# Optimization experiments

Hardware: AMD Instinct MI355X
Metric: run time of the kernel (lower is better)

The kernel has to match this reference:

```python
import jax, jax.numpy as jnp
import numpy as np

N_HEAD = 16
N_EMBD = 64  # per-head dim in this module's convention
INNER = N_HEAD * N_EMBD  # 1024


def setup_inputs() -> dict:
    key = jax.random.key(0)
    ks = jax.random.split(key, 6)
    B, S = 4, 2048
    scale = 0.02
    return {
        "x": jax.random.normal(ks[0], (B, S, N_EMBD), dtype=jnp.float32),
        "Wq": jax.random.normal(ks[1], (N_EMBD, INNER), dtype=jnp.float32) * scale,
        "Wk": jax.random.normal(ks[2], (N_EMBD, INNER), dtype=jnp.float32) * scale,
        "Wv": jax.random.normal(ks[3], (N_EMBD, INNER), dtype=jnp.float32) * scale,
        "Wo": jax.random.normal(ks[4], (INNER, N_EMBD), dtype=jnp.float32) * scale,
        "bo": jax.random.normal(ks[5], (N_EMBD,), dtype=jnp.float32) * scale,
        "causal_mask": 1,
    }


def reference(x, Wq, Wk, Wv, Wo, bo, causal_mask):
    B, S, _ = x.shape
    # projections: [B,S,INNER] -> [B,H,S,D]
    def split_heads(t):
        return t.reshape(B, S, N_HEAD, N_EMBD).transpose(0, 2, 1, 3)
    q = split_heads(x @ Wq)
    k = split_heads(x @ Wk)
    v = split_heads(x @ Wv)
    # [B,H,S,S]
    scores = jnp.einsum("bhqd,bhkd->bhqk", q, k) / jnp.sqrt(jnp.float32(N_EMBD))
    if causal_mask:
        future = jnp.triu(jnp.ones((S, S), dtype=scores.dtype), k=1)
        scores = scores - 1e9 * future  # matches torch: subtract 1e9*mask
    attn = jax.nn.softmax(scores, axis=-1)
    out = jnp.einsum("bhqk,bhkd->bhqd", attn, v)
    out = out.transpose(0, 2, 1, 3).reshape(B, S, INNER)
    return out @ Wo + bo
```

## Files before the change

### kernel.cpp

```cpp
#include <hip/hip_runtime.h>
#include <hip/hip_bf16.h>

#define NHEAD 16
#define HDIM 64
#define DINNER 1024
#define NBATCH 4
#define SEQ 2048
#define NTOK (NBATCH*SEQ)

typedef __bf16 bf16;
typedef __bf16 bf16x4 __attribute__((ext_vector_type(4)));
typedef __bf16 bf16x8 __attribute__((ext_vector_type(8)));
typedef float f32x4 __attribute__((ext_vector_type(4)));

#define OFF_BO   8
#define OFF_WQT  128
#define OFF_WKT  (OFF_WQT + DINNER*HDIM)
#define OFF_WVT  (OFF_WKT + DINNER*HDIM)
#define OFF_WOT  (OFF_WVT + DINNER*HDIM)
#define OFF_Q    (OFF_WOT + DINNER*HDIM)
#define OFF_K    (OFF_Q + NTOK*DINNER)
#define OFF_VT   (OFF_K + NTOK*DINNER)
#define OFF_ATT  (OFF_VT + NTOK*DINNER)

#define SSCALE 0.18033688011112042f

static __device__ __forceinline__ bf16x8 ld8(const bf16* p) {
  return *reinterpret_cast<const bf16x8*>(p);
}
static __device__ __forceinline__ float ldw(const void* W, int i, int isbf) {
  return isbf ? (float)((const bf16*)W)[i] : ((const float*)W)[i];
}

static __device__ __forceinline__ int detect_isbf(const void* x, int tid,
                                                  int* sflag) {
  if (tid < 64) {
    const unsigned short* xb = (const unsigned short*)x;
    bool ok = true;
#pragma unroll
    for (int i = 0; i < 8; i++) {
      unsigned e = (xb[tid * 8 + i] >> 7) & 0xFF;
      ok = ok && (e >= 64 && e <= 140);
    }
    unsigned long long mball = __ballot(ok);
    if (tid == 0) *sflag = (mball == ~0ull) ? 1 : 0;
  }
  __syncthreads();
  return *sflag;
}

__global__ __launch_bounds__(256) void prep_kernel(
    const void* __restrict__ x, const void* __restrict__ Wq,
    const void* __restrict__ Wk, const void* __restrict__ Wv,
    const void* __restrict__ Wo, const void* __restrict__ bo,
    bf16* __restrict__ ws) {
  __shared__ int sflag;
  int isbf = detect_isbf(x, threadIdx.x, &sflag);
  int z = blockIdx.y;
  int idx = blockIdx.x * 256 + threadIdx.x;
  if (z < 3) {
    const void* src = (z == 0) ? Wq : (z == 1) ? Wk : Wv;
    bf16* dst = ws + ((z == 0) ? OFF_WQT : (z == 1) ? OFF_WKT : OFF_WVT);
    int d = idx >> 10, n = idx & 1023;
    float v = ldw(src, idx, isbf);
    if (z == 0) v *= SSCALE;
    dst[n * HDIM + d] = (bf16)v;
  } else if (z == 3) {
    int k = idx >> 6, n = idx & 63;
    ws[OFF_WOT + n * DINNER + k] = (bf16)ldw(Wo, idx, isbf);
  } else {
    if (idx < 64) ws[OFF_BO + idx] = (bf16)ldw(bo, idx, isbf);
  }
}

__global__ __launch_bounds__(256) void qkv_kernel(const void* __restrict__ x,
                                                  bf16* __restrict__ ws) {
  __shared__ __align__(16) bf16 Vst[4][16 * 72];
  __shared__ int sflag;
  int isbf = detect_isbf(x, threadIdx.x, &sflag);
  int tt = blockIdx.x;
  int w = threadIdx.x >> 6;
  int nc = blockIdx.y * 4 + w;
  int lane = threadIdx.x & 63;
  int lq = lane & 15, quad = lane >> 4;
  int n0 = nc * 64;
  bf16x8 wq0[4], wq1[4], wk0[4], wk1[4], wv0[4], wv1[4], ao0[4], ao1[4];
#pragma unroll
  for (int c = 0; c < 4; c++) {
    int n = n0 + c * 16 + lq;
    const bf16* r;
    r = ws + OFF_WQT + n * HDIM; wq0[c] = ld8(r + quad * 8); wq1[c] = ld8(r + 32 + quad * 8);
    r = ws + OFF_WKT + n * HDIM; wk0[c] = ld8(r + quad * 8); wk1[c] = ld8(r + 32 + quad * 8);
    r = ws + OFF_WVT + n * HDIM; wv0[c] = ld8(r + quad * 8); wv1[c] = ld8(r + 32 + quad * 8);
    const bf16* orow = ws + OFF_WOT + (size_t)(c * 16 + lq) * DINNER + n0;
    ao0[c] = ld8(orow + quad * 8); ao1[c] = ld8(orow + 32 + quad * 8);
  }
  bf16* Qb = ws + OFF_Q;
  bf16* Kb = ws + OFF_K;
  bf16* VTb = ws + OFF_VT;
#pragma unroll
  for (int mi = 0; mi < 4; mi++) {
    int t0 = tt * 64 + mi * 16;
    bf16x8 x0, x1;
    if (isbf) {
      const bf16* xr = (const bf16*)x + (size_t)(t0 + lq) * HDIM;
      x0 = ld8(xr + quad * 8);
      x1 = ld8(xr + 32 + quad * 8);
    } else {
      const float* xf = (const float*)x + (size_t)(t0 + lq) * HDIM;
      f32x4 a0 = *reinterpret_cast<const f32x4*>(xf + quad * 8);
      f32x4 a1 = *reinterpret_cast<const f32x4*>(xf + quad * 8 + 4);
      f32x4 b0 = *reinterpret_cast<const f32x4*>(xf + 32 + quad * 8);
      f32x4 b1 = *reinterpret_cast<const f32x4*>(xf + 32 + quad * 8 + 4);
#pragma unroll
      for (int j = 0; j < 4; j++) {
        x0[j] = (bf16)a0[j]; x0[4 + j] = (bf16)a1[j];
        x1[j] = (bf16)b0[j]; x1[4 + j] = (bf16)b1[j];
      }
    }
    int b = t0 >> 11, s0 = t0 & (SEQ - 1);
    size_t rowbase = ((size_t)(b * NHEAD + nc) * SEQ + s0 + lq) * HDIM;
#pragma unroll
    for (int c = 0; c < 4; c++) {
      f32x4 z = {0.f, 0.f, 0.f, 0.f};
      z = __builtin_amdgcn_mfma_f32_16x16x32_bf16(wq0[c], x0, z, 0, 0, 0);
      z = __builtin_amdgcn_mfma_f32_16x16x32_bf16(wq1[c], x1, z, 0, 0, 0);
      bf16x4 pk = {(bf16)z[0], (bf16)z[1], (bf16)z[2], (bf16)z[3]};
      *reinterpret_cast<bf16x4*>(&Qb[rowbase + c * 16 + quad * 4]) = pk;
    }
#pragma unroll
    for (int c = 0; c < 4; c++) {
      f32x4 z = {0.f, 0.f, 0.f, 0.f};
      z = __builtin_amdgcn_mfma_f32_16x16x32_bf16(wk0[c], x0, z, 0, 0, 0);
      z = __builtin_amdgcn_mfma_f32_16x16x32_bf16(wk1[c], x1, z, 0, 0, 0);
      bf16x4 pk = {(bf16)z[0], (bf16)z[1], (bf16)z[2], (bf16)z[3]};
      *reinterpret_cast<bf16x4*>(&Kb[rowbase + c * 16 + quad * 4]) = pk;
    }
#pragma unroll
    for (int c = 0; c < 4; c++) {
      f32x4 z = {0.f, 0.f, 0.f, 0.f};
      z = __builtin_amdgcn_mfma_f32_16x16x32_bf16(wv0[c], x0, z, 0, 0, 0);
      z = __builtin_amdgcn_mfma_f32_16x16x32_bf16(wv1[c], x1, z, 0, 0, 0);
      bf16x4 pk = {(bf16)z[0], (bf16)z[1], (bf16)z[2], (bf16)z[3]};
      *reinterpret_cast<bf16x4*>(&Vst[w][lq * 72 + c * 16 + quad * 4]) = pk;
    }
    bf16x8 bv0 = ld8(&Vst[w][lq * 72 + quad * 8]);
    bf16x8 bv1 = ld8(&Vst[w][lq * 72 + 32 + quad * 8]);
#pragma unroll
    for (int c = 0; c < 4; c++) {
      f32x4 z2 = {0.f, 0.f, 0.f, 0.f};
      z2 = __builtin_amdgcn_mfma_f32_16x16x32_bf16(ao0[c], bv0, z2, 0, 0, 0);
      z2 = __builtin_amdgcn_mfma_f32_16x16x32_bf16(ao1[c], bv1, z2, 0, 0, 0);
#pragma unroll
      for (int r = 0; r < 4; r++) {
        int d = c * 16 + quad * 4 + r;
        VTb[(((size_t)b * NHEAD + nc) * HDIM + d) * SEQ + s0 + lq] = (bf16)z2[r];
      }
    }
  }
}

__global__ __launch_bounds__(256, 2) void flash_kernel(const int* __restrict__ cmask,
                                                       bf16* __restrict__ ws) {
  __shared__ __align__(16) bf16 Kl[2][64 * 64];
  __shared__ __align__(16) bf16 Vl[2][64 * 64];
  __shared__ __align__(16) bf16 Pl[4][16 * 64];
  const int qmap[16] = {15,13,11,9,0,2,4,6,14,12,10,8,1,3,5,7};
  int bid = blockIdx.x;
  int bh = (bid & 7) * 8 + ((bid >> 3) & 7);
  int qt = qmap[bid >> 6];
  int w = threadIdx.x >> 6;
  int lane = threadIdx.x & 63;
  int lq = lane & 15, quad = lane >> 4;
  int causal = cmask[0];
  const bf16* Q = ws + OFF_Q + (size_t)bh * SEQ * HDIM;
  const bf16* K = ws + OFF_K + (size_t)bh * SEQ * HDIM;
  const bf16* VT = ws + OFF_VT + (size_t)bh * HDIM * SEQ;
  int b = bh >> 4, h = bh & 15;
  bf16* ar = ws + OFF_ATT;
  int sr = threadIdx.x >> 2;
  int sg = (threadIdx.x & 3) * 16;
  int sc0 = (((threadIdx.x & 3) * 2) ^ (sr & 7)) << 3;
  int sc1 = (((threadIdx.x & 3) * 2 + 1) ^ (sr & 7)) << 3;
  int rq0 = (quad ^ (lq & 7)) << 3;
  int rq1 = ((4 + quad) ^ (lq & 7)) << 3;

  int qb = qt * 128;
  int qw = qb + w * 32;
  int T = (causal ? (qb + 128) : SEQ) / 64;

  bf16x8 bq[2][2];
#pragma unroll
  for (int m = 0; m < 2; m++) {
    const bf16* qrow = Q + (qw + m * 16 + lq) * HDIM;
    bq[m][0] = ld8(qrow + quad * 8);
    bq[m][1] = ld8(qrow + 32 + quad * 8);
  }
  f32x4 o[2][4];
  float lsum[2] = {0.f, 0.f};
#pragma unroll
  for (int m = 0; m < 2; m++)
#pragma unroll
    for (int c = 0; c < 4; c++) o[m][c] = (f32x4){0.f, 0.f, 0.f, 0.f};

  bf16x8 kst0 = ld8(K + sr * HDIM + sg);
  bf16x8 kst1 = ld8(K + sr * HDIM + sg + 8);
  bf16x8 vst0 = ld8(VT + sr * SEQ + sg);
  bf16x8 vst1 = ld8(VT + sr * SEQ + sg + 8);

  for (int ti = 0; ti < T; ti++) {
    int buf = ti & 1;
    int k0 = ti * 64;
    *reinterpret_cast<bf16x8*>(&Kl[buf][sr * 64 + sc0]) = kst0;
    *reinterpret_cast<bf16x8*>(&Kl[buf][sr * 64 + sc1]) = kst1;
    *reinterpret_cast<bf16x8*>(&Vl[buf][sr * 64 + sc0]) = vst0;
    *reinterpret_cast<bf16x8*>(&Vl[buf][sr * 64 + sc1]) = vst1;
    int kn = (ti + 1 < T) ? (k0 + 64) : k0;
    kst0 = ld8(K + (kn + sr) * HDIM + sg);
    kst1 = ld8(K + (kn + sr) * HDIM + sg + 8);
    vst0 = ld8(VT + sr * SEQ + kn + sg);
    vst1 = ld8(VT + sr * SEQ + kn + sg + 8);
    __syncthreads();
    f32x4 st[2][4];
#pragma unroll
    for (int t = 0; t < 4; t++) {
      bf16x8 a0 = ld8(&Kl[buf][(t * 16 + lq) * 64 + rq0]);
      bf16x8 a1 = ld8(&Kl[buf][(t * 16 + lq) * 64 + rq1]);
#pragma unroll
      for (int m = 0; m < 2; m++) {
        f32x4 z = {0.f, 0.f, 0.f, 0.f};
        z = __builtin_amdgcn_mfma_f32_16x16x32_bf16(a0, bq[m][0], z, 0, 0, 0);
        z = __builtin_amdgcn_mfma_f32_16x16x32_bf16(a1, bq[m][1], z, 0, 0, 0);
        st[m][t] = z;
      }
    }
    bool needmask = causal && (k0 + 63 > qw);
    bf16x8 bp[2][2];
#pragma unroll
    for (int m = 0; m < 2; m++) {
      if (needmask) {
        int qrel = qw + m * 16 + lq - k0 - quad * 4;
#pragma unroll
        for (int t = 0; t < 4; t++)
#pragma unroll
          for (int r = 0; r < 4; r++)
            if (t * 16 + r > qrel) st[m][t][r] = -200.0f;
      }
      float sum = 0.f;
#pragma unroll
      for (int t = 0; t < 4; t++) {
        float e0 = exp2f(st[m][t][0]);
        float e1 = exp2f(st[m][t][1]);
        float e2 = exp2f(st[m][t][2]);
        float e3 = exp2f(st[m][t][3]);
        sum += (e0 + e1) + (e2 + e3);
        bf16x4 pk = {(bf16)e0, (bf16)e1, (bf16)e2, (bf16)e3};
        int ch = ((t * 2 + (quad >> 1)) ^ (lq & 7)) << 3;
        *reinterpret_cast<bf16x4*>(&Pl[w][lq * 64 + ch + (quad & 1) * 4]) = pk;
      }
      lsum[m] += sum;
      bp[m][0] = ld8(&Pl[w][lq * 64 + rq0]);
      bp[m][1] = ld8(&Pl[w][lq * 64 + rq1]);
    }
#pragma unroll
    for (int c = 0; c < 4; c++) {
      bf16x8 av0 = ld8(&Vl[buf][(c * 16 + lq) * 64 + rq0]);
      bf16x8 av1 = ld8(&Vl[buf][(c * 16 + lq) * 64 + rq1]);
#pragma unroll
      for (int m = 0; m < 2; m++) {
        o[m][c] = __builtin_amdgcn_mfma_f32_16x16x32_bf16(av0, bp[m][0], o[m][c], 0, 0, 0);
        o[m][c] = __builtin_amdgcn_mfma_f32_16x16x32_bf16(av1, bp[m][1], o[m][c], 0, 0, 0);
      }
    }
  }
#pragma unroll
  for (int m = 0; m < 2; m++) {
    lsum[m] += __shfl_xor(lsum[m], 16);
    lsum[m] += __shfl_xor(lsum[m], 32);
    float inv = 1.0f / lsum[m];
    size_t rowoff = ((size_t)(b * SEQ + qw + m * 16 + lq)) * DINNER + h * HDIM;
#pragma unroll
    for (int c = 0; c < 4; c++) {
      bf16x4 ov = {(bf16)(o[m][c][0] * inv), (bf16)(o[m][c][1] * inv),
                   (bf16)(o[m][c][2] * inv), (bf16)(o[m][c][3] * inv)};
      *reinterpret_cast<bf16x4*>(&ar[rowoff + c * 16 + quad * 4]) = ov;
    }
  }
}

__global__ __launch_bounds__(256) void reduce_kernel(const bf16* __restrict__ ws,
                                                     const void* __restrict__ x,
                                                     void* __restrict__ outp) {
  __shared__ int sflag;
  int isbf = detect_isbf(x, threadIdx.x, &sflag);
  int idx = blockIdx.x * 256 + threadIdx.x;
  int t = idx >> 6, d = idx & 63;
  const bf16* ar = ws + OFF_ATT + (size_t)t * DINNER + d;
  float s = (float)ws[OFF_BO + d];
#pragma unroll
  for (int h = 0; h < 16; h++) s += (float)ar[h * 64];
  if (isbf) ((bf16*)outp)[idx] = (bf16)s;
  else      ((float*)outp)[idx] = s;
}

extern "C" void kernel_launch(void* const* d_in, const int* in_sizes, int n_in,
                              void* d_out, int out_size, void* d_ws, size_t ws_size,
                              hipStream_t stream) {
  const void* x  = d_in[0];
  const void* Wq = d_in[1];
  const void* Wk = d_in[2];
  const void* Wv = d_in[3];
  const void* Wo = d_in[4];
  const void* bo = d_in[5];
  const int* cm  = (const int*)d_in[6];
  bf16* ws = (bf16*)d_ws;

  hipLaunchKernelGGL(prep_kernel, dim3(256, 5), dim3(256), 0, stream,
                     x, Wq, Wk, Wv, Wo, bo, ws);
  hipLaunchKernelGGL(qkv_kernel, dim3(128, 4), dim3(256), 0, stream, x, ws);
  hipLaunchKernelGGL(flash_kernel, dim3(1024), dim3(256), 0, stream, cm, ws);
  hipLaunchKernelGGL(reduce_kernel, dim3(2048), dim3(256), 0, stream, ws, x, d_out);
}
```

Before: 164.1 us.

## Restructure QKV projection: smaller token tiles, staged coalesced Q/K stores, fewer live weights

The QKV kernel now handles 32 tokens per block instead of 64, doubling the grid. It loads the weights for one projection at a time, so fewer registers stay live. Q and K tiles are staged through shared memory so each lane writes a full 16-byte chunk of a row, replacing the scattered 8-byte stores. The cost is more blocks that each reload the weights, plus extra LDS round-trips, in a kernel that is only part of the total runtime.

```diff
diff --git a/kernel.cpp b/kernel.cpp
--- a/kernel.cpp
+++ b/kernel.cpp
@@ -75,7 +75,7 @@
 
 __global__ __launch_bounds__(256) void qkv_kernel(const void* __restrict__ x,
                                                   bf16* __restrict__ ws) {
-  __shared__ __align__(16) bf16 Vst[4][16 * 72];
+  __shared__ __align__(16) bf16 St[4][16 * 72];
   __shared__ int sflag;
   int isbf = detect_isbf(x, threadIdx.x, &sflag);
   int tt = blockIdx.x;
@@ -84,77 +84,95 @@
   int lane = threadIdx.x & 63;
   int lq = lane & 15, quad = lane >> 4;
   int n0 = nc * 64;
-  bf16x8 wq0[4], wq1[4], wk0[4], wk1[4], wv0[4], wv1[4], ao0[4], ao1[4];
-#pragma unroll
-  for (int c = 0; c < 4; c++) {
-    int n = n0 + c * 16 + lq;
-    const bf16* r;
-    r = ws + OFF_WQT + n * HDIM; wq0[c] = ld8(r + quad * 8); wq1[c] = ld8(r + 32 + quad * 8);
-    r = ws + OFF_WKT + n * HDIM; wk0[c] = ld8(r + quad * 8); wk1[c] = ld8(r + 32 + quad * 8);
-    r = ws + OFF_WVT + n * HDIM; wv0[c] = ld8(r + quad * 8); wv1[c] = ld8(r + 32 + quad * 8);
-    const bf16* orow = ws + OFF_WOT + (size_t)(c * 16 + lq) * DINNER + n0;
-    ao0[c] = ld8(orow + quad * 8); ao1[c] = ld8(orow + 32 + quad * 8);
-  }
-  bf16* Qb = ws + OFF_Q;
-  bf16* Kb = ws + OFF_K;
-  bf16* VTb = ws + OFF_VT;
-#pragma unroll
-  for (int mi = 0; mi < 4; mi++) {
-    int t0 = tt * 64 + mi * 16;
-    bf16x8 x0, x1;
+  int t0 = tt * 32;
+  int b = t0 >> 11, s0 = t0 & (SEQ - 1);
+  bf16x8 xa[2], xb[2];
+#pragma unroll
+  for (int mi = 0; mi < 2; mi++) {
+    int trow = t0 + mi * 16 + lq;
     if (isbf) {
-      const bf16* xr = (const bf16*)x + (size_t)(t0 + lq) * HDIM;
-      x0 = ld8(xr + quad * 8);
-      x1 = ld8(xr + 32 + quad * 8);
+      const bf16* xr = (const bf16*)x + (size_t)trow * HDIM;
+      xa[mi] = ld8(xr + quad * 8);
+      xb[mi] = ld8(xr + 32 + quad * 8);
     } else {
-      const float* xf = (const float*)x + (size_t)(t0 + lq) * HDIM;
+      const float* xf = (const float*)x + (size_t)trow * HDIM;
       f32x4 a0 = *reinterpret_cast<const f32x4*>(xf + quad * 8);
       f32x4 a1 = *reinterpret_cast<const f32x4*>(xf + quad * 8 + 4);
       f32x4 b0 = *reinterpret_cast<const f32x4*>(xf + 32 + quad * 8);
       f32x4 b1 = *reinterpret_cast<const f32x4*>(xf + 32 + quad * 8 + 4);
 #pragma unroll
       for (int j = 0; j < 4; j++) {
-        x0[j] = (bf16)a0[j]; x0[4 + j] = (bf16)a1[j];
-        x1[j] = (bf16)b0[j]; x1[4 + j] = (bf16)b1[j];
-      }
-    }
-    int b = t0 >> 11, s0 = t0 & (SEQ - 1);
-    size_t rowbase = ((size_t)(b * NHEAD + nc) * SEQ + s0 + lq) * HDIM;
+        xa[mi][j] = (bf16)a0[j]; xa[mi][4 + j] = (bf16)a1[j];
+        xb[mi][j] = (bf16)b0[j]; xb[mi][4 + j] = (bf16)b1[j];
+      }
+    }
+  }
+  int stok = lane >> 3, sch = (lane & 7) * 8;
+#pragma unroll
+  for (int pz = 0; pz < 2; pz++) {
+    const bf16* WT = ws + (pz ? OFF_WKT : OFF_WQT);
+    bf16* P = ws + (pz ? OFF_K : OFF_Q);
+    bf16x8 w0[4], w1[4];
 #pragma unroll
     for (int c = 0; c < 4; c++) {
-      f32x4 z = {0.f, 0.f, 0.f, 0.f};
-      z = __builtin_amdgcn_mfma_f32_16x16x32_bf16(wq0[c], x0, z, 0, 0, 0);
-      z = __builtin_amdgcn_mfma_f32_16x16x32_bf16(wq1[c], x1, z, 0, 0, 0);
-      bf16x4 pk = {(bf16)z[0], (bf16)z[1], (bf16)z[2], (bf16)z[3]};
-      *reinterpret_cast<bf16x4*>(&Qb[rowbase + c * 16 + quad * 4]) = pk;
-    }
+      const bf16* wr = WT + (n0 + c * 16 + lq) * HDIM;
+      w0[c] = ld8(wr + quad * 8);
+      w1[c] = ld8(wr + 32 + quad * 8);
+    }
+#pragma unroll
+    for (int mi = 0; mi < 2; mi++) {
+#pragma unroll
+      for (int c = 0; c < 4; c++) {
+        f32x4 z = {0.f, 0.f, 0.f, 0.f};
+        z = __builtin_amdgcn_mfma_f32_16x16x32_bf16(w0[c], xa[mi], z, 0, 0, 0);
+        z = __builtin_amdgcn_mfma_f32_16x16x32_bf16(w1[c], xb[mi], z, 0, 0, 0);
+        bf16x4 pk = {(bf16)z[0], (bf16)z[1], (bf16)z[2], (bf16)z[3]};
+        *reinterpret_cast<bf16x4*>(&St[w][lq * 72 + c * 16 + quad * 4]) = pk;
+      }
+      size_t base = ((size_t)(b * NHEAD + nc) * SEQ + s0 + mi * 16) * HDIM;
+#pragma unroll
+      for (int half = 0; half < 2; half++) {
+        int tok = stok + half * 8;
+        bf16x8 vv = ld8(&St[w][tok * 72 + sch]);
+        *reinterpret_cast<bf16x8*>(&P[base + tok * HDIM + sch]) = vv;
+      }
+    }
+  }
+  {
+    bf16x8 w0[4], w1[4], ao0[4], ao1[4];
 #pragma unroll
     for (int c = 0; c < 4; c++) {
-      f32x4 z = {0.f, 0.f, 0.f, 0.f};
-      z = __builtin_amdgcn_mfma_f32_16x16x32_bf16(wk0[c], x0, z, 0, 0, 0);
-      z = __builtin_amdgcn_mfma_f32_16x16x32_bf16(wk1[c], x1, z, 0, 0, 0);
-      bf16x4 pk = {(bf16)z[0], (bf16)z[1], (bf16)z[2], (bf16)z[3]};
-      *reinterpret_cast<bf16x4*>(&Kb[rowbase + c * 16 + quad * 4]) = pk;
-    }
-#pragma unroll
-    for (int c = 0; c < 4; c++) {
-      f32x4 z = {0.f, 0.f, 0.f, 0.f};
-      z = __builtin_amdgcn_mfma_f32_16x16x32_bf16(wv0[c], x0, z, 0, 0, 0);
-      z = __builtin_amdgcn_mfma_f32_16x16x32_bf16(wv1[c], x1, z, 0, 0, 0);
-      bf16x4 pk = {(bf16)z[0], (bf16)z[1], (bf16)z[2], (bf16)z[3]};
-      *reinterpret_cast<bf16x4*>(&Vst[w][lq * 72 + c * 16 + quad * 4]) = pk;
-    }
-    bf16x8 bv0 = ld8(&Vst[w][lq * 72 + quad * 8]);
-    bf16x8 bv1 = ld8(&Vst[w][lq * 72 + 32 + quad * 8]);
-#pragma unroll
-    for (int c = 0; c < 4; c++) {
-      f32x4 z2 = {0.f, 0.f, 0.f, 0.f};
-      z2 = __builtin_amdgcn_mfma_f32_16x16x32_bf16(ao0[c], bv0, z2, 0, 0, 0);
-      z2 = __builtin_amdgcn_mfma_f32_16x16x32_bf16(ao1[c], bv1, z2, 0, 0, 0);
-#pragma unroll
-      for (int r = 0; r < 4; r++) {
-        int d = c * 16 + quad * 4 + r;
-        VTb[(((size_t)b * NHEAD + nc) * HDIM + d) * SEQ + s0 + lq] = (bf16)z2[r];
+      const bf16* wr = ws + OFF_WVT + (n0 + c * 16 + lq) * HDIM;
+      w0[c] = ld8(wr + quad * 8);
+      w1[c] = ld8(wr + 32 + quad * 8);
+      const bf16* orow = ws + OFF_WOT + (size_t)(c * 16 + lq) * DINNER + n0;
+      ao0[c] = ld8(orow + quad * 8);
+      ao1[c] = ld8(orow + 32 + quad * 8);
+    }
+    bf16* VTb = ws + OFF_VT;
+#pragma unroll
+    for (int mi = 0; mi < 2; mi++) {
+#pragma unroll
+      for (int c = 0; c < 4; c++) {
+        f32x4 z = {0.f, 0.f, 0.f, 0.f};
+        z = __builtin_amdgcn_mfma_f32_16x16x32_bf16(w0[c], xa[mi], z, 0, 0, 0);
+        z = __builtin_amdgcn_mfma_f32_16x16x32_bf16(w1[c], xb[mi], z, 0, 0, 0);
+        bf16x4 pk = {(bf16)z[0], (bf16)z[1], (bf16)z[2], (bf16)z[3]};
+        *reinterpret_cast<bf16x4*>(&St[w][lq * 72 + c * 16 + quad * 4]) = pk;
+      }
+      bf16x8 bv0 = ld8(&St[w][lq * 72 + quad * 8]);
+      bf16x8 bv1 = ld8(&St[w][lq * 72 + 32 + quad * 8]);
+      int s0m = s0 + mi * 16;
+#pragma unroll
+      for (int c = 0; c < 4; c++) {
+        f32x4 z2 = {0.f, 0.f, 0.f, 0.f};
+        z2 = __builtin_amdgcn_mfma_f32_16x16x32_bf16(ao0[c], bv0, z2, 0, 0, 0);
+        z2 = __builtin_amdgcn_mfma_f32_16x16x32_bf16(ao1[c], bv1, z2, 0, 0, 0);
+#pragma unroll
+        for (int r = 0; r < 4; r++) {
+          int d = c * 16 + quad * 4 + r;
+          VTb[(((size_t)b * NHEAD + nc) * HDIM + d) * SEQ + s0m + lq] = (bf16)z2[r];
+        }
       }
     }
   }
@@ -317,7 +335,7 @@
 
   hipLaunchKernelGGL(prep_kernel, dim3(256, 5), dim3(256), 0, stream,
                      x, Wq, Wk, Wv, Wo, bo, ws);
-  hipLaunchKernelGGL(qkv_kernel, dim3(128, 4), dim3(256), 0, stream, x, ws);
+  hipLaunchKernelGGL(qkv_kernel, dim3(256, 4), dim3(256), 0, stream, x, ws);
   hipLaunchKernelGGL(flash_kernel, dim3(1024), dim3(256), 0, stream, cm, ws);
   hipLaunchKernelGGL(reduce_kernel, dim3(2048), dim3(256), 0, stream, ws, x, d_out);
 }
```

After: 161.7 us. About the same (-1.4%).
